# Optimization experiments

Measured on AMD Instinct MI355X. Metric: run time of the kernel, lower is better.

The kernel has to match this reference:

```python
import jax, jax.numpy as jnp
import numpy as np

EPS = 1e-8
SOFTEN = 1.0
COLOR_NORM = 1.0


def setup_inputs() -> dict:
    key = jax.random.key(0)
    k1, k2, k3, k4 = jax.random.split(key, 4)
    B, C, H, W = 16, 3, 224, 224
    K, HID = 64, 256
    img = jax.random.uniform(k1, (B, C, H, W), dtype=jnp.float32)
    W1 = jax.random.normal(k2, (HID, C), dtype=jnp.float32) * 0.1
    b1 = jax.random.normal(k3, (HID,), dtype=jnp.float32) * 0.1
    W2 = jax.random.normal(k4, (K, HID), dtype=jnp.float32) * 0.1
    return {"img": img, "W1": W1, "b1": b1, "W2": W2}


def reference(img, W1, b1, W2):
    # color_mask: 1x1 conv (3->256) + ReLU + 1x1 conv (256->K, no bias)
    h = jax.nn.relu(jnp.einsum('bchw,oc->bohw', img, W1) + b1[None, :, None, None])
    logits = jnp.einsum('bohw,ko->bkhw', h, W2)
    # Softmax2d == softmax over channel dim; soften=1
    m = jax.nn.softmax(SOFTEN * logits, axis=1)  # (B,K,H,W)
    # training=True path: soft weighted palette.
    # (img[:,:,None]*m[:,None]).sum(spatial) contracted directly via einsum
    # to avoid materializing the (B,3,K,H,W) broadcast tensor.
    num = jnp.einsum('bchw,bkhw->bck', img, m)          # (B,3,K)
    den = jnp.sum(m, axis=(2, 3))                        # (B,K)
    palette = num / (den[:, None, :] + EPS) / COLOR_NORM  # (B,3,K)
    # color_jitter=0 -> jitter_palette == palette
    transformed_img = jnp.einsum('bkhw,bck->bchw', m, palette)
    # match torch shape (B,3,K,1,1) for palette output
    return transformed_img, m, palette[:, :, :, None, None]
```

## Files before the change

kernel.cpp:

```cpp
#include <hip/hip_runtime.h>
#include <hip/hip_bf16.h>

#define BATCH 16
#define HW 50176
#define HID 256
#define K 64

#define OUT_T_OFF 0
#define OUT_M_OFF 2408448
#define OUT_P_OFF 53788672

#define WS_DEN 0
#define WS_NUM 1024
#define WS_W1P 4096
#define WS_W2B 5120

typedef short bf16x8 __attribute__((ext_vector_type(8)));
typedef float f32x4  __attribute__((ext_vector_type(4)));

static __device__ __forceinline__ short f2bf(float x) {
    union { __hip_bfloat16 h; short s; } u;
    u.h = __float2bfloat16(x);
    return u.s;
}

__global__ __launch_bounds__(256) void colorcnn_prep(
    const float* __restrict__ W1, const float* __restrict__ b1,
    const float* __restrict__ W2, float* __restrict__ wsf,
    float4* __restrict__ w1p, ushort* __restrict__ w2b)
{
    const int t = threadIdx.x;
#pragma unroll
    for (int q = 0; q < 16; ++q) wsf[q * 256 + t] = 0.f;
    w1p[t] = make_float4(W1[3 * t], W1[3 * t + 1], W1[3 * t + 2], b1[t]);
#pragma unroll
    for (int q = 0; q < 64; ++q) {
        const int i = q * 256 + t;
        w2b[i] = (ushort)f2bf(W2[i]);
    }
}

__global__ __launch_bounds__(256) void colorcnn_mlp_softmax(
    const float* __restrict__ img, const float4* __restrict__ w1p,
    const ushort* __restrict__ w2b, float* __restrict__ m_out,
    float* __restrict__ den_ws, float* __restrict__ num_ws)
{
    __shared__ int4 lds[2304];
    __shared__ float sred[4][256];

    const int t = threadIdx.x;
    const int4* w2b16 = (const int4*)w2b;
#pragma unroll
    for (int q = 0; q < 8; ++q) {
        const int i = t + q * 256;
        const int n = i >> 5, s = i & 31;
        lds[n * 32 + (s ^ (n & 7))] = w2b16[i];
    }
    lds[2048 + (t ^ ((t >> 3) & 3))] = ((const int4*)w1p)[t];
    __syncthreads();

    const int b    = blockIdx.y;
    const int pb   = blockIdx.x * 128;
    const int w    = t >> 6;
    const int lane = t & 63;
    const int l15  = lane & 15;
    const int lg   = lane >> 4;

    const float* ip = img + (size_t)b * 3 * HW;
    const int px0 = pb + w * 32 + l15;
    const int px1 = px0 + 16;
    const float r0 = ip[px0], g0 = ip[HW + px0], u0 = ip[2 * HW + px0];
    const float r1 = ip[px1], g1 = ip[HW + px1], u1 = ip[2 * HW + px1];

    f32x4 acc[2][4];
#pragma unroll
    for (int mi = 0; mi < 2; ++mi)
#pragma unroll
        for (int ni = 0; ni < 4; ++ni)
            acc[mi][ni] = (f32x4){0.f, 0.f, 0.f, 0.f};

#pragma unroll
    for (int c = 0; c < 8; ++c) {
        bf16x8 a0, a1;
#pragma unroll
        for (int j = 0; j < 8; ++j) {
            const int hid = c * 32 + lg * 8 + j;
            const float4 wv = *(const float4*)&lds[2048 + (hid ^ lg)];
            float t0 = fmaf(r0, wv.x, fmaf(g0, wv.y, fmaf(u0, wv.z, wv.w)));
            float t1 = fmaf(r1, wv.x, fmaf(g1, wv.y, fmaf(u1, wv.z, wv.w)));
            a0[j] = f2bf(fmaxf(t0, 0.f));
            a1[j] = f2bf(fmaxf(t1, 0.f));
        }
#pragma unroll
        for (int ni = 0; ni < 4; ++ni) {
            const int n = ni * 16 + l15;
            const bf16x8 bf = *(const bf16x8*)&lds[n * 32 + (((c * 4 + lg) ^ (n & 7)))];
            acc[0][ni] = __builtin_amdgcn_mfma_f32_16x16x32_bf16(a0, bf, acc[0][ni], 0, 0, 0);
            acc[1][ni] = __builtin_amdgcn_mfma_f32_16x16x32_bf16(a1, bf, acc[1][ni], 0, 0, 0);
        }
    }

#pragma unroll
    for (int mi = 0; mi < 2; ++mi) {
#pragma unroll
        for (int reg = 0; reg < 4; ++reg) {
            float v0 = acc[mi][0][reg], v1 = acc[mi][1][reg];
            float v2 = acc[mi][2][reg], v3 = acc[mi][3][reg];
            float mx = fmaxf(fmaxf(v0, v1), fmaxf(v2, v3));
            mx = fmaxf(mx, __shfl_xor(mx, 1));
            mx = fmaxf(mx, __shfl_xor(mx, 2));
            mx = fmaxf(mx, __shfl_xor(mx, 4));
            mx = fmaxf(mx, __shfl_xor(mx, 8));
            v0 = __expf(v0 - mx); v1 = __expf(v1 - mx);
            v2 = __expf(v2 - mx); v3 = __expf(v3 - mx);
            float s = (v0 + v1) + (v2 + v3);
            s += __shfl_xor(s, 1);
            s += __shfl_xor(s, 2);
            s += __shfl_xor(s, 4);
            s += __shfl_xor(s, 8);
            const float inv = 1.f / s;
            acc[mi][0][reg] = v0 * inv; acc[mi][1][reg] = v1 * inv;
            acc[mi][2][reg] = v2 * inv; acc[mi][3][reg] = v3 * inv;
        }
    }

    float* mo = m_out + (size_t)b * K * HW + pb + w * 32;
#pragma unroll
    for (int mi = 0; mi < 2; ++mi)
#pragma unroll
        for (int ni = 0; ni < 4; ++ni) {
            const int n = ni * 16 + l15;
            *(f32x4*)&mo[(size_t)n * HW + mi * 16 + lg * 4] = acc[mi][ni];
        }

    f32x4 rC[2], gC[2], uC[2];
#pragma unroll
    for (int mi = 0; mi < 2; ++mi) {
        const int pxb = pb + w * 32 + mi * 16 + lg * 4;
        rC[mi] = *(const f32x4*)&ip[pxb];
        gC[mi] = *(const f32x4*)&ip[HW + pxb];
        uC[mi] = *(const f32x4*)&ip[2 * HW + pxb];
    }
    float red[16];
#pragma unroll
    for (int ni = 0; ni < 4; ++ni) {
        float d = 0.f, nr = 0.f, ng = 0.f, nb = 0.f;
#pragma unroll
        for (int mi = 0; mi < 2; ++mi) {
#pragma unroll
            for (int reg = 0; reg < 4; ++reg) {
                const float mv = acc[mi][ni][reg];
                d += mv;
                nr = fmaf(rC[mi][reg], mv, nr);
                ng = fmaf(gC[mi][reg], mv, ng);
                nb = fmaf(uC[mi][reg], mv, nb);
            }
        }
        red[ni] = d; red[4 + ni] = nr; red[8 + ni] = ng; red[12 + ni] = nb;
    }
#pragma unroll
    for (int i = 0; i < 16; ++i) {
        red[i] += __shfl_xor(red[i], 16);
        red[i] += __shfl_xor(red[i], 32);
    }
    if (lg == 0) {
#pragma unroll
        for (int ni = 0; ni < 4; ++ni) {
            const int n = ni * 16 + l15;
            sred[w][n]       = red[ni];
            sred[w][64 + n]  = red[4 + ni];
            sred[w][128 + n] = red[8 + ni];
            sred[w][192 + n] = red[12 + ni];
        }
    }
    __syncthreads();
    {
        const int q = t >> 6, n = t & 63;
        const float v = sred[0][t] + sred[1][t] + sred[2][t] + sred[3][t];
        if (q == 0) atomicAdd(&den_ws[b * K + n], v);
        else        atomicAdd(&num_ws[(b * 3 + (q - 1)) * K + n], v);
    }
}

__global__ __launch_bounds__(256) void colorcnn_palette(
    const float* __restrict__ den_ws, const float* __restrict__ num_ws,
    float* __restrict__ pal_out)
{
    const int i = blockIdx.x * 256 + threadIdx.x;
    if (i >= BATCH * K) return;
    const int b = i >> 6;
    const int k = i & 63;
    const float dv = den_ws[i] + 1e-8f;
#pragma unroll
    for (int c = 0; c < 3; ++c)
        pal_out[b * 3 * K + c * K + k] = num_ws[(b * 3 + c) * K + k] / dv;
}

__global__ __launch_bounds__(256) void colorcnn_reconstruct(
    const float* __restrict__ m, const float* __restrict__ pal,
    float* __restrict__ t_out)
{
    __shared__ float pl[192];
    const int b = blockIdx.x / 49;
    const int p = (blockIdx.x % 49) * 1024 + threadIdx.x * 4;

    if (threadIdx.x < 192) pl[threadIdx.x] = pal[b * 3 * K + threadIdx.x];
    __syncthreads();

    const float* mp = m + (size_t)b * K * HW + p;
    f32x4 ar = {0.f, 0.f, 0.f, 0.f}, ag = ar, ab = ar;
#pragma unroll
    for (int k = 0; k < K; ++k) {
        const f32x4 mv = *(const f32x4*)&mp[(size_t)k * HW];
        const float pr = pl[k], pg = pl[K + k], pu = pl[2 * K + k];
#pragma unroll
        for (int j = 0; j < 4; ++j) {
            ar[j] = fmaf(mv[j], pr, ar[j]);
            ag[j] = fmaf(mv[j], pg, ag[j]);
            ab[j] = fmaf(mv[j], pu, ab[j]);
        }
    }
    float* to = t_out + (size_t)b * 3 * HW + p;
    *(f32x4*)&to[0]      = ar;
    *(f32x4*)&to[HW]     = ag;
    *(f32x4*)&to[2 * HW] = ab;
}

extern "C" void kernel_launch(void* const* d_in, const int* in_sizes, int n_in,
                              void* d_out, int out_size, void* d_ws, size_t ws_size,
                              hipStream_t stream) {
    const float* img = (const float*)d_in[0];
    const float* W1  = (const float*)d_in[1];
    const float* b1  = (const float*)d_in[2];
    const float* W2  = (const float*)d_in[3];

    float* out   = (float*)d_out;
    float* t_out = out + OUT_T_OFF;
    float* m_out = out + OUT_M_OFF;
    float* p_out = out + OUT_P_OFF;

    float*  wsf    = (float*)d_ws;
    float*  den_ws = wsf + WS_DEN;
    float*  num_ws = wsf + WS_NUM;
    float4* w1p    = (float4*)(wsf + WS_W1P);
    ushort* w2b    = (ushort*)(wsf + WS_W2B);

    colorcnn_prep<<<1, 256, 0, stream>>>(W1, b1, W2, wsf, w1p, w2b);
    colorcnn_mlp_softmax<<<dim3(HW / 128, BATCH), 256, 0, stream>>>(img, w1p, w2b, m_out, den_ws, num_ws);
    colorcnn_palette<<<4, 256, 0, stream>>>(den_ws, num_ws, p_out);
    colorcnn_reconstruct<<<BATCH * 49, 256, 0, stream>>>(m_out, p_out, t_out);
}
```

Measured before the change: 132.8 us.

## Double pixels per block, drop softmax max-subtraction, parallelize weight prep

Each wave now handles 64 pixels instead of 32, so the LDS weight staging per block is amortized over twice as many pixels and there are half as many atomics. The softmax no longer subtracts the row max before exponentiating, which removes the shuffle reduction but risks overflow for large logits. The prep kernel is split across 8 blocks to convert W2 to bf16 in parallel. Keeping 16 accumulators per lane raises register pressure and may lower occupancy.

```diff
diff --git a/kernel.cpp b/kernel.cpp
--- a/kernel.cpp
+++ b/kernel.cpp
@@ -30,12 +30,14 @@
     float4* __restrict__ w1p, ushort* __restrict__ w2b)
 {
     const int t = threadIdx.x;
-#pragma unroll
-    for (int q = 0; q < 16; ++q) wsf[q * 256 + t] = 0.f;
-    w1p[t] = make_float4(W1[3 * t], W1[3 * t + 1], W1[3 * t + 2], b1[t]);
-#pragma unroll
-    for (int q = 0; q < 64; ++q) {
-        const int i = q * 256 + t;
+    if (blockIdx.x == 0) {
+#pragma unroll
+        for (int q = 0; q < 16; ++q) wsf[q * 256 + t] = 0.f;
+        w1p[t] = make_float4(W1[3 * t], W1[3 * t + 1], W1[3 * t + 2], b1[t]);
+    }
+#pragma unroll
+    for (int q = 0; q < 8; ++q) {
+        const int i = (blockIdx.x * 8 + q) * 256 + t;
         w2b[i] = (ushort)f2bf(W2[i]);
     }
 }
@@ -60,36 +62,44 @@
     __syncthreads();
 
     const int b    = blockIdx.y;
-    const int pb   = blockIdx.x * 128;
+    const int pb   = blockIdx.x * 256;
     const int w    = t >> 6;
     const int lane = t & 63;
     const int l15  = lane & 15;
     const int lg   = lane >> 4;
+    const int pwb  = pb + w * 64;
 
     const float* ip = img + (size_t)b * 3 * HW;
-    const int px0 = pb + w * 32 + l15;
-    const int px1 = px0 + 16;
-    const float r0 = ip[px0], g0 = ip[HW + px0], u0 = ip[2 * HW + px0];
-    const float r1 = ip[px1], g1 = ip[HW + px1], u1 = ip[2 * HW + px1];
-
-    f32x4 acc[2][4];
-#pragma unroll
-    for (int mi = 0; mi < 2; ++mi)
+
+    float rr[4], gg[4], uu[4];
+#pragma unroll
+    for (int s = 0; s < 4; ++s) {
+        const int px = pwb + s * 16 + l15;
+        rr[s] = ip[px]; gg[s] = ip[HW + px]; uu[s] = ip[2 * HW + px];
+    }
+
+    f32x4 acc[4][4];
+#pragma unroll
+    for (int s = 0; s < 4; ++s)
 #pragma unroll
         for (int ni = 0; ni < 4; ++ni)
-            acc[mi][ni] = (f32x4){0.f, 0.f, 0.f, 0.f};
+            acc[s][ni] = (f32x4){0.f, 0.f, 0.f, 0.f};
 
 #pragma unroll
     for (int c = 0; c < 8; ++c) {
-        bf16x8 a0, a1;
+        bf16x8 a0, a1, a2, a3;
 #pragma unroll
         for (int j = 0; j < 8; ++j) {
             const int hid = c * 32 + lg * 8 + j;
             const float4 wv = *(const float4*)&lds[2048 + (hid ^ lg)];
-            float t0 = fmaf(r0, wv.x, fmaf(g0, wv.y, fmaf(u0, wv.z, wv.w)));
-            float t1 = fmaf(r1, wv.x, fmaf(g1, wv.y, fmaf(u1, wv.z, wv.w)));
+            float t0 = fmaf(rr[0], wv.x, fmaf(gg[0], wv.y, fmaf(uu[0], wv.z, wv.w)));
+            float t1 = fmaf(rr[1], wv.x, fmaf(gg[1], wv.y, fmaf(uu[1], wv.z, wv.w)));
+            float t2 = fmaf(rr[2], wv.x, fmaf(gg[2], wv.y, fmaf(uu[2], wv.z, wv.w)));
+            float t3 = fmaf(rr[3], wv.x, fmaf(gg[3], wv.y, fmaf(uu[3], wv.z, wv.w)));
             a0[j] = f2bf(fmaxf(t0, 0.f));
             a1[j] = f2bf(fmaxf(t1, 0.f));
+            a2[j] = f2bf(fmaxf(t2, 0.f));
+            a3[j] = f2bf(fmaxf(t3, 0.f));
         }
 #pragma unroll
         for (int ni = 0; ni < 4; ++ni) {
@@ -97,63 +107,60 @@
             const bf16x8 bf = *(const bf16x8*)&lds[n * 32 + (((c * 4 + lg) ^ (n & 7)))];
             acc[0][ni] = __builtin_amdgcn_mfma_f32_16x16x32_bf16(a0, bf, acc[0][ni], 0, 0, 0);
             acc[1][ni] = __builtin_amdgcn_mfma_f32_16x16x32_bf16(a1, bf, acc[1][ni], 0, 0, 0);
-        }
-    }
-
-#pragma unroll
-    for (int mi = 0; mi < 2; ++mi) {
+            acc[2][ni] = __builtin_amdgcn_mfma_f32_16x16x32_bf16(a2, bf, acc[2][ni], 0, 0, 0);
+            acc[3][ni] = __builtin_amdgcn_mfma_f32_16x16x32_bf16(a3, bf, acc[3][ni], 0, 0, 0);
+        }
+    }
+
+#pragma unroll
+    for (int s = 0; s < 4; ++s) {
 #pragma unroll
         for (int reg = 0; reg < 4; ++reg) {
-            float v0 = acc[mi][0][reg], v1 = acc[mi][1][reg];
-            float v2 = acc[mi][2][reg], v3 = acc[mi][3][reg];
-            float mx = fmaxf(fmaxf(v0, v1), fmaxf(v2, v3));
-            mx = fmaxf(mx, __shfl_xor(mx, 1));
-            mx = fmaxf(mx, __shfl_xor(mx, 2));
-            mx = fmaxf(mx, __shfl_xor(mx, 4));
-            mx = fmaxf(mx, __shfl_xor(mx, 8));
-            v0 = __expf(v0 - mx); v1 = __expf(v1 - mx);
-            v2 = __expf(v2 - mx); v3 = __expf(v3 - mx);
-            float s = (v0 + v1) + (v2 + v3);
-            s += __shfl_xor(s, 1);
-            s += __shfl_xor(s, 2);
-            s += __shfl_xor(s, 4);
-            s += __shfl_xor(s, 8);
-            const float inv = 1.f / s;
-            acc[mi][0][reg] = v0 * inv; acc[mi][1][reg] = v1 * inv;
-            acc[mi][2][reg] = v2 * inv; acc[mi][3][reg] = v3 * inv;
-        }
-    }
-
-    float* mo = m_out + (size_t)b * K * HW + pb + w * 32;
-#pragma unroll
-    for (int mi = 0; mi < 2; ++mi)
+            float v0 = __expf(acc[s][0][reg]);
+            float v1 = __expf(acc[s][1][reg]);
+            float v2 = __expf(acc[s][2][reg]);
+            float v3 = __expf(acc[s][3][reg]);
+            float sm = (v0 + v1) + (v2 + v3);
+            sm += __shfl_xor(sm, 1);
+            sm += __shfl_xor(sm, 2);
+            sm += __shfl_xor(sm, 4);
+            sm += __shfl_xor(sm, 8);
+            const float inv = 1.f / sm;
+            acc[s][0][reg] = v0 * inv; acc[s][1][reg] = v1 * inv;
+            acc[s][2][reg] = v2 * inv; acc[s][3][reg] = v3 * inv;
+        }
+    }
+
+    float* mo = m_out + (size_t)b * K * HW + pwb;
+#pragma unroll
+    for (int s = 0; s < 4; ++s)
 #pragma unroll
         for (int ni = 0; ni < 4; ++ni) {
             const int n = ni * 16 + l15;
-            *(f32x4*)&mo[(size_t)n * HW + mi * 16 + lg * 4] = acc[mi][ni];
-        }
-
-    f32x4 rC[2], gC[2], uC[2];
-#pragma unroll
-    for (int mi = 0; mi < 2; ++mi) {
-        const int pxb = pb + w * 32 + mi * 16 + lg * 4;
-        rC[mi] = *(const f32x4*)&ip[pxb];
-        gC[mi] = *(const f32x4*)&ip[HW + pxb];
-        uC[mi] = *(const f32x4*)&ip[2 * HW + pxb];
+            *(f32x4*)&mo[(size_t)n * HW + s * 16 + lg * 4] = acc[s][ni];
+        }
+
+    f32x4 rC[4], gC[4], uC[4];
+#pragma unroll
+    for (int s = 0; s < 4; ++s) {
+        const int pxb = pwb + s * 16 + lg * 4;
+        rC[s] = *(const f32x4*)&ip[pxb];
+        gC[s] = *(const f32x4*)&ip[HW + pxb];
+        uC[s] = *(const f32x4*)&ip[2 * HW + pxb];
     }
     float red[16];
 #pragma unroll
     for (int ni = 0; ni < 4; ++ni) {
         float d = 0.f, nr = 0.f, ng = 0.f, nb = 0.f;
 #pragma unroll
-        for (int mi = 0; mi < 2; ++mi) {
+        for (int s = 0; s < 4; ++s) {
 #pragma unroll
             for (int reg = 0; reg < 4; ++reg) {
-                const float mv = acc[mi][ni][reg];
+                const float mv = acc[s][ni][reg];
                 d += mv;
-                nr = fmaf(rC[mi][reg], mv, nr);
-                ng = fmaf(gC[mi][reg], mv, ng);
-                nb = fmaf(uC[mi][reg], mv, nb);
+                nr = fmaf(rC[s][reg], mv, nr);
+                ng = fmaf(gC[s][reg], mv, ng);
+                nb = fmaf(uC[s][reg], mv, nb);
             }
         }
         red[ni] = d; red[4 + ni] = nr; red[8 + ni] = ng; red[12 + ni] = nb;
@@ -245,8 +252,8 @@
     float4* w1p    = (float4*)(wsf + WS_W1P);
     ushort* w2b    = (ushort*)(wsf + WS_W2B);
 
-    colorcnn_prep<<<1, 256, 0, stream>>>(W1, b1, W2, wsf, w1p, w2b);
-    colorcnn_mlp_softmax<<<dim3(HW / 128, BATCH), 256, 0, stream>>>(img, w1p, w2b, m_out, den_ws, num_ws);
+    colorcnn_prep<<<8, 256, 0, stream>>>(W1, b1, W2, wsf, w1p, w2b);
+    colorcnn_mlp_softmax<<<dim3(HW / 256, BATCH), 256, 0, stream>>>(img, w1p, w2b, m_out, den_ws, num_ws);
     colorcnn_palette<<<4, 256, 0, stream>>>(den_ws, num_ws, p_out);
     colorcnn_reconstruct<<<BATCH * 49, 256, 0, stream>>>(m_out, p_out, t_out);
 }
```

After: 136.0 us. 2.4% more time.
